# Performance work log

Measured on AMD Instinct MI355X. Metric: run time of the kernel, lower is better.

## Reference

```python
import jax, jax.numpy as jnp
import numpy as np

NEG_FILL = -9.0e15


def setup_inputs() -> dict:
    key = jax.random.key(0)
    k1, k2 = jax.random.split(key)
    z1 = jax.random.normal(k1, (4096, 256), dtype=jnp.float32)
    z2 = jax.random.normal(k2, (4096, 256), dtype=jnp.float32)
    return {"z1": z1, "z2": z2}


def reference(z1, z2, temperature=0.5):
    B = z1.shape[0]
    z = jnp.concatenate([z1, z2], axis=0)          # [2B, D]
    # cosine similarity == dot product of L2-normalized rows (torch eps=1e-8)
    norm = jnp.maximum(jnp.linalg.norm(z, axis=1, keepdims=True), 1e-8)
    zn = z / norm                                   # [2B, D]
    sim = (zn @ zn.T) / temperature                 # [2B, 2B]
    N = 2 * B
    eye = jnp.eye(N, dtype=bool)
    sim = jnp.where(eye, NEG_FILL, sim)
    idx = jnp.arange(N)
    # positives: (i, i+B mod 2B) -> diag(sim, B) then diag(sim, -B)
    pos_sim = sim[idx, (idx + B) % N]               # [2B]
    loss = -pos_sim + jax.nn.logsumexp(sim, axis=1)
    return jnp.mean(loss)
```

## Files before the change

### kernel.cpp

```cpp
#include <hip/hip_runtime.h>
#include <hip/hip_bf16.h>


typedef __attribute__((ext_vector_type(4))) float f32x4;
typedef __attribute__((ext_vector_type(8))) int i32x8;

#define N_TOT 8192
#define B_HALF 4096
#define D_DIM 256
#define JSPLIT 16
#define JCOLS 512
#define NSTEP 8
#define SCL_PRE 1.6986436f
#define RES_SCALE 0.6931471805599453f
#define S4 0x7B7B7B7B

__device__ inline float fexp2(float x) {
#if __has_builtin(__builtin_amdgcn_exp2f)
  return __builtin_amdgcn_exp2f(x);
#else
  return exp2f(x);
#endif
}

__device__ inline unsigned enc4(float v) {
  float av = fabsf(v);
  unsigned c = (av >= 0.25f) + (av >= 0.75f) + (av >= 1.25f) + (av >= 1.75f) +
               (av >= 2.5f) + (av >= 3.5f) + (av >= 5.0f);
  return c | ((v < 0.f) ? 8u : 0u);
}

__device__ inline i32x8 ld16z(const char* p) {
  int4 lo = *reinterpret_cast<const int4*>(p);
  i32x8 r = {lo.x, lo.y, lo.z, lo.w, 0, 0, 0, 0};
  return r;
}

__global__ __launch_bounds__(256) void nrm_kernel(const float* __restrict__ z1,
                                                  const float* __restrict__ z2,
                                                  unsigned short* __restrict__ zn4) {
  int row = blockIdx.x * 4 + (threadIdx.x >> 6);
  int lane = threadIdx.x & 63;
  const float* src = (row < B_HALF) ? (z1 + (size_t)row * D_DIM)
                                    : (z2 + (size_t)(row - B_HALF) * D_DIM);
  f32x4 v = *reinterpret_cast<const f32x4*>(src + lane * 4);
  float ss = v.x * v.x + v.y * v.y + v.z * v.z + v.w * v.w;
#pragma unroll
  for (int m = 32; m >= 1; m >>= 1) ss += __shfl_xor(ss, m);
  float inv = (SCL_PRE * 16.0f) / fmaxf(sqrtf(ss), 1e-8f);
  unsigned n0 = enc4(v.x * inv), n1 = enc4(v.y * inv);
  unsigned n2 = enc4(v.z * inv), n3 = enc4(v.w * inv);
  zn4[(size_t)row * 64 + lane] =
      (unsigned short)(n0 | (n1 << 4) | (n2 << 8) | (n3 << 12));
}

__global__ __launch_bounds__(256, 4) void gram_kernel(const unsigned short* __restrict__ zn4,
                                                      float* __restrict__ psum,
                                                      float* __restrict__ ppos) {
  __shared__ __align__(16) char bt[2 * 64 * 128];
  const int tid = threadIdx.x;
  const int w = tid >> 6, l = tid & 63;
  const int lm = l & 15, hh = l >> 4;
  const int r0w = blockIdx.x * 128 + w * 32;
  const int jbase = blockIdx.y * JCOLS;
  const char* znb = reinterpret_cast<const char*>(zn4);

  auto stage = [&](int s, int bi) {
    const char* gs = znb + (size_t)(jbase + s * 64) * 128;
    char* base = bt + bi * 8192 + w * 1024;
#pragma unroll
    for (int q = 0; q < 2; ++q) {
      int rloc = q * 32 + w * 8 + (l >> 3);
      int d = l & 7;
      const char* g = gs + (size_t)rloc * 128 + ((d ^ (rloc & 7)) << 4);
      __builtin_amdgcn_global_load_lds(
          (const __attribute__((address_space(1))) void*)g,
          (__attribute__((address_space(3))) void*)(base + q * 4096), 16, 0, 0);
    }
  };

  stage(0, 0);

  i32x8 a[2][2];
#pragma unroll
  for (int rf = 0; rf < 2; ++rf)
#pragma unroll
    for (int sl = 0; sl < 2; ++sl)
      a[rf][sl] = ld16z(znb + (size_t)(r0w + rf * 16 + lm) * 128 + sl * 64 + hh * 16);

  float sume[2][4];
#pragma unroll
  for (int rf = 0; rf < 2; ++rf)
#pragma unroll
    for (int t = 0; t < 4; ++t) sume[rf][t] = 0.f;

  const int swz = (lm & 7) << 4;

  f32x4 acA[2], acB[2];
  int pjtb = -1;

  auto readS = [&](const char* bp, int jt, int sl, i32x8& b) {
    const char* row = bp + (jt * 16 + lm) * 128;
    int cs = (sl * 64 + hh * 16) ^ swz;
    b = ld16z(row + cs);
  };

  auto epilogue = [&](const f32x4 (&pa)[2], int jtb) {
#pragma unroll
    for (int rf = 0; rf < 2; ++rf) {
      const int itb = r0w + rf * 16;
      const bool dg = (itb == jtb);
      const bool ps = ((itb ^ B_HALF) == jtb);
      if (dg | ps) {
#pragma unroll
        for (int t = 0; t < 4; ++t) {
          float sv = pa[rf][t];
          float e = fexp2(sv);
          bool self = (lm == hh * 4 + t);
          if (dg && self) e = 0.f;
          sume[rf][t] += e;
          if (ps && self) ppos[itb + hh * 4 + t] = sv * RES_SCALE;
        }
      } else {
#pragma unroll
        for (int t = 0; t < 4; ++t) sume[rf][t] += fexp2(pa[rf][t]);
      }
    }
  };

  auto mfma2 = [&](f32x4 (&acc)[2], const i32x8& b, int sl) {
    __builtin_amdgcn_s_setprio(1);
#pragma unroll
    for (int rf = 0; rf < 2; ++rf)
      acc[rf] = __builtin_amdgcn_mfma_scale_f32_16x16x128_f8f6f4(
          a[rf][sl], b, acc[rf], 4, 4, 0, S4, 0, S4);
    __builtin_amdgcn_s_setprio(0);
  };

  for (int s = 0; s < NSTEP; ++s) {
    __syncthreads();
    if (s + 1 < NSTEP) stage(s + 1, (s + 1) & 1);
    const char* bp = bt + (s & 1) * 8192;

    i32x8 b[8];
#pragma unroll
    for (int u = 0; u < 8; ++u) readS(bp, u >> 1, u & 1, b[u]);

#pragma unroll
    for (int jt = 0; jt < 4; ++jt) {
      f32x4(&acc)[2] = (jt & 1) ? acB : acA;
      f32x4(&prev)[2] = (jt & 1) ? acA : acB;

      if (pjtb >= 0) epilogue(prev, pjtb);
#pragma unroll
      for (int rf = 0; rf < 2; ++rf) acc[rf] = (f32x4){0.f, 0.f, 0.f, 0.f};
      mfma2(acc, b[jt * 2], 0);
      mfma2(acc, b[jt * 2 + 1], 1);
      pjtb = jbase + s * 64 + jt * 16;
    }
  }
  epilogue(acB, pjtb);

#pragma unroll
  for (int rf = 0; rf < 2; ++rf)
#pragma unroll
    for (int t = 0; t < 4; ++t) {
      float v = sume[rf][t];
#pragma unroll
      for (int m = 1; m < 16; m <<= 1) v += __shfl_xor(v, m);
      if (lm == 0) psum[(size_t)blockIdx.y * N_TOT + r0w + rf * 16 + hh * 4 + t] = v;
    }
}

__global__ __launch_bounds__(256) void fin1_kernel(const float* __restrict__ psum,
                                                   const float* __restrict__ ppos,
                                                   float* __restrict__ partial) {
  int i = blockIdx.x * 256 + threadIdx.x;
  float se = 0.f;
#pragma unroll
  for (int s = 0; s < JSPLIT; ++s) se += psum[(size_t)s * N_TOT + i];
  float acc = logf(se) - ppos[i];
#pragma unroll
  for (int m = 32; m >= 1; m >>= 1) acc += __shfl_xor(acc, m);
  __shared__ float red[4];
  if ((threadIdx.x & 63) == 0) red[threadIdx.x >> 6] = acc;
  __syncthreads();
  if (threadIdx.x == 0) partial[blockIdx.x] = red[0] + red[1] + red[2] + red[3];
}

__global__ void fin2_kernel(const float* __restrict__ partial, float* __restrict__ out) {
  float v = (threadIdx.x < 32) ? partial[threadIdx.x] : 0.f;
#pragma unroll
  for (int m = 32; m >= 1; m >>= 1) v += __shfl_xor(v, m);
  if (threadIdx.x == 0) out[0] = v / (float)N_TOT;
}

extern "C" void kernel_launch(void* const* d_in, const int* in_sizes, int n_in,
                              void* d_out, int out_size, void* d_ws, size_t ws_size,
                              hipStream_t stream) {
  const float* z1 = (const float*)d_in[0];
  const float* z2 = (const float*)d_in[1];
  float* out = (float*)d_out;
  char* ws = (char*)d_ws;

  unsigned short* zn4 = (unsigned short*)ws;
  float* psum = (float*)(ws + (size_t)N_TOT * 128);
  float* ppos = psum + (size_t)JSPLIT * N_TOT;
  float* partial = ppos + N_TOT;

  nrm_kernel<<<N_TOT / 4, 256, 0, stream>>>(z1, z2, zn4);
  gram_kernel<<<dim3(N_TOT / 128, JSPLIT), 256, 0, stream>>>(zn4, psum, ppos);
  fin1_kernel<<<N_TOT / 256, 256, 0, stream>>>(psum, ppos, partial);
  fin2_kernel<<<1, 64, 0, stream>>>(partial, out);
}
```

Measured before the change: 30.08 us.

## Exploit Gram matrix symmetry by computing only upper-triangular tiles

Restructures the gram kernel to compute only upper-triangular 128x256 tiles of the symmetric similarity matrix. Each exp value is added to both the row sum and a column sum, with column partials reduced through shared memory. The grid becomes a 1D triangular enumeration, and the finalize step gathers row and column partials. This roughly halves the MFMA and exp work, at the cost of extra column reductions, LDS traffic, a triangular index mapping, and uneven handling of the diagonal blocks.

New measurement: 43.18 us. 43.6% more time.

```diff
diff --git a/kernel.cpp b/kernel.cpp
--- a/kernel.cpp
+++ b/kernel.cpp
@@ -8,9 +8,10 @@
 #define N_TOT 8192
 #define B_HALF 4096
 #define D_DIM 256
-#define JSPLIT 16
-#define JCOLS 512
-#define NSTEP 8
+#define NROWP 32
+#define NCOLP 64
+#define NSTEP 4
+#define NBLK 1056
 #define SCL_PRE 1.6986436f
 #define RES_SCALE 0.6931471805599453f
 #define S4 0x7B7B7B7B
@@ -55,19 +56,32 @@
 }
 
 __global__ __launch_bounds__(256, 4) void gram_kernel(const unsigned short* __restrict__ zn4,
-                                                      float* __restrict__ psum,
+                                                      float* __restrict__ rowp,
+                                                      float* __restrict__ colp,
                                                       float* __restrict__ ppos) {
   __shared__ __align__(16) char bt[2 * 64 * 128];
+  __shared__ float colLDS[4][256];
   const int tid = threadIdx.x;
   const int w = tid >> 6, l = tid & 63;
   const int lm = l & 15, hh = l >> 4;
-  const int r0w = blockIdx.x * 128 + w * 32;
-  const int jbase = blockIdx.y * JCOLS;
+
+  const int L = blockIdx.x;
+  int p = (int)((65.0f - sqrtf(4225.0f - 4.0f * (float)L)) * 0.5f);
+  if (p < 0) p = 0;
+  while (p < 32 && (p + 1) * (65 - (p + 1)) <= L) ++p;
+  while (p > 0 && p * (65 - p) > L) --p;
+  int r = L - p * (65 - p);
+  int bi, bj;
+  if (r < 32 - p) { bi = 2 * p; bj = p + r; }
+  else            { bi = 2 * p + 1; bj = p + (r - (32 - p)); }
+
+  const int r0w = bi * 128 + w * 32;
+  const int jbase = bj * 256;
   const char* znb = reinterpret_cast<const char*>(zn4);
 
-  auto stage = [&](int s, int bi) {
+  auto stage = [&](int s, int bfi) {
     const char* gs = znb + (size_t)(jbase + s * 64) * 128;
-    char* base = bt + bi * 8192 + w * 1024;
+    char* base = bt + bfi * 8192 + w * 1024;
 #pragma unroll
     for (int q = 0; q < 2; ++q) {
       int rloc = q * 32 + w * 8 + (l >> 3);
@@ -96,70 +110,120 @@
 
   const int swz = (lm & 7) << 4;
 
-  f32x4 acA[2], acB[2];
-  int pjtb = -1;
-
   auto readS = [&](const char* bp, int jt, int sl, i32x8& b) {
     const char* row = bp + (jt * 16 + lm) * 128;
     int cs = (sl * 64 + hh * 16) ^ swz;
     b = ld16z(row + cs);
   };
 
-  auto epilogue = [&](const f32x4 (&pa)[2], int jtb) {
-#pragma unroll
-    for (int rf = 0; rf < 2; ++rf) {
-      const int itb = r0w + rf * 16;
-      const bool dg = (itb == jtb);
-      const bool ps = ((itb ^ B_HALF) == jtb);
-      if (dg | ps) {
+  if (bj > (bi >> 1)) {
+    f32x4 acA[2], acB[2];
+    int pjtb = -1, pcol = 0;
+
+    auto epiF = [&](const f32x4 (&pa)[2], int jtb, int pc) {
+      float csum = 0.f;
+#pragma unroll
+      for (int rf = 0; rf < 2; ++rf) {
+        const int itb = r0w + rf * 16;
+        const bool ps = ((itb ^ B_HALF) == jtb);
 #pragma unroll
         for (int t = 0; t < 4; ++t) {
           float sv = pa[rf][t];
           float e = fexp2(sv);
-          bool self = (lm == hh * 4 + t);
-          if (dg && self) e = 0.f;
           sume[rf][t] += e;
-          if (ps && self) ppos[itb + hh * 4 + t] = sv * RES_SCALE;
-        }
-      } else {
-#pragma unroll
-        for (int t = 0; t < 4; ++t) sume[rf][t] += fexp2(pa[rf][t]);
+          csum += e;
+          if (ps && (lm == hh * 4 + t)) {
+            ppos[itb + hh * 4 + t] = sv * RES_SCALE;
+            ppos[jtb + lm] = sv * RES_SCALE;
+          }
+        }
       }
-    }
-  };
-
-  auto mfma2 = [&](f32x4 (&acc)[2], const i32x8& b, int sl) {
-    __builtin_amdgcn_s_setprio(1);
-#pragma unroll
-    for (int rf = 0; rf < 2; ++rf)
-      acc[rf] = __builtin_amdgcn_mfma_scale_f32_16x16x128_f8f6f4(
-          a[rf][sl], b, acc[rf], 4, 4, 0, S4, 0, S4);
-    __builtin_amdgcn_s_setprio(0);
-  };
-
-  for (int s = 0; s < NSTEP; ++s) {
-    __syncthreads();
-    if (s + 1 < NSTEP) stage(s + 1, (s + 1) & 1);
-    const char* bp = bt + (s & 1) * 8192;
-
-    i32x8 b[8];
-#pragma unroll
-    for (int u = 0; u < 8; ++u) readS(bp, u >> 1, u & 1, b[u]);
-
-#pragma unroll
-    for (int jt = 0; jt < 4; ++jt) {
-      f32x4(&acc)[2] = (jt & 1) ? acB : acA;
-      f32x4(&prev)[2] = (jt & 1) ? acA : acB;
-
-      if (pjtb >= 0) epilogue(prev, pjtb);
-#pragma unroll
-      for (int rf = 0; rf < 2; ++rf) acc[rf] = (f32x4){0.f, 0.f, 0.f, 0.f};
-      mfma2(acc, b[jt * 2], 0);
-      mfma2(acc, b[jt * 2 + 1], 1);
-      pjtb = jbase + s * 64 + jt * 16;
+      csum += __shfl_xor(csum, 16);
+      csum += __shfl_xor(csum, 32);
+      if (hh == 0) colLDS[w][pc + lm] = csum;
+    };
+
+    for (int s = 0; s < NSTEP; ++s) {
+      __syncthreads();
+      if (s + 1 < NSTEP) stage(s + 1, (s + 1) & 1);
+      const char* bp = bt + (s & 1) * 8192;
+      i32x8 b[8];
+#pragma unroll
+      for (int u = 0; u < 8; ++u) readS(bp, u >> 1, u & 1, b[u]);
+
+#pragma unroll
+      for (int jt = 0; jt < 4; ++jt) {
+        f32x4(&acc)[2] = (jt & 1) ? acB : acA;
+        f32x4(&prev)[2] = (jt & 1) ? acA : acB;
+        if (pjtb >= 0) epiF(prev, pjtb, pcol);
+#pragma unroll
+        for (int rf = 0; rf < 2; ++rf) acc[rf] = (f32x4){0.f, 0.f, 0.f, 0.f};
+        __builtin_amdgcn_s_setprio(1);
+#pragma unroll
+        for (int rf = 0; rf < 2; ++rf) {
+          acc[rf] = __builtin_amdgcn_mfma_scale_f32_16x16x128_f8f6f4(
+              a[rf][0], b[jt * 2], acc[rf], 4, 4, 0, S4, 0, S4);
+          acc[rf] = __builtin_amdgcn_mfma_scale_f32_16x16x128_f8f6f4(
+              a[rf][1], b[jt * 2 + 1], acc[rf], 4, 4, 0, S4, 0, S4);
+        }
+        __builtin_amdgcn_s_setprio(0);
+        pjtb = jbase + s * 64 + jt * 16;
+        pcol = s * 64 + jt * 16;
+      }
+    }
+    epiF(acB, pjtb, pcol);
+  } else {
+    for (int s = 0; s < NSTEP; ++s) {
+      __syncthreads();
+      if (s + 1 < NSTEP) stage(s + 1, (s + 1) & 1);
+      const char* bp = bt + (s & 1) * 8192;
+      i32x8 b[8];
+#pragma unroll
+      for (int u = 0; u < 8; ++u) readS(bp, u >> 1, u & 1, b[u]);
+
+#pragma unroll
+      for (int jt = 0; jt < 4; ++jt) {
+        const int jtb = jbase + s * 64 + jt * 16;
+        float csum = 0.f;
+        f32x4 acc[2];
+#pragma unroll
+        for (int rf = 0; rf < 2; ++rf) acc[rf] = (f32x4){0.f, 0.f, 0.f, 0.f};
+#pragma unroll
+        for (int rf = 0; rf < 2; ++rf) {
+          const int itb = r0w + rf * 16;
+          if (jtb >= itb) {
+            acc[rf] = __builtin_amdgcn_mfma_scale_f32_16x16x128_f8f6f4(
+                a[rf][0], b[jt * 2], acc[rf], 4, 4, 0, S4, 0, S4);
+            acc[rf] = __builtin_amdgcn_mfma_scale_f32_16x16x128_f8f6f4(
+                a[rf][1], b[jt * 2 + 1], acc[rf], 4, 4, 0, S4, 0, S4);
+          }
+        }
+#pragma unroll
+        for (int rf = 0; rf < 2; ++rf) {
+          const int itb = r0w + rf * 16;
+          if (jtb < itb) continue;
+          if (jtb == itb) {
+#pragma unroll
+            for (int t = 0; t < 4; ++t) {
+              float e = fexp2(acc[rf][t]);
+              if (lm == hh * 4 + t) e = 0.f;
+              sume[rf][t] += e;
+            }
+          } else {
+#pragma unroll
+            for (int t = 0; t < 4; ++t) {
+              float e = fexp2(acc[rf][t]);
+              sume[rf][t] += e;
+              csum += e;
+            }
+          }
+        }
+        csum += __shfl_xor(csum, 16);
+        csum += __shfl_xor(csum, 32);
+        if (hh == 0) colLDS[w][s * 64 + jt * 16 + lm] = csum;
+      }
     }
   }
-  epilogue(acB, pjtb);
 
 #pragma unroll
   for (int rf = 0; rf < 2; ++rf)
@@ -168,24 +232,30 @@
       float v = sume[rf][t];
 #pragma unroll
       for (int m = 1; m < 16; m <<= 1) v += __shfl_xor(v, m);
-      if (lm == 0) psum[(size_t)blockIdx.y * N_TOT + r0w + rf * 16 + hh * 4 + t] = v;
-    }
-}
-
-__global__ __launch_bounds__(256) void fin1_kernel(const float* __restrict__ psum,
+      if (lm == 0) rowp[(size_t)bj * N_TOT + r0w + rf * 16 + hh * 4 + t] = v;
+    }
+
+  __syncthreads();
+  float cs = colLDS[0][tid] + colLDS[1][tid] + colLDS[2][tid] + colLDS[3][tid];
+  colp[(size_t)bi * N_TOT + jbase + tid] = cs;
+}
+
+__global__ __launch_bounds__(256) void fin1_kernel(const float* __restrict__ rowp,
+                                                   const float* __restrict__ colp,
                                                    const float* __restrict__ ppos,
                                                    float* __restrict__ partial) {
-  int i = blockIdx.x * 256 + threadIdx.x;
+  const int bx = blockIdx.x;
+  const int i = bx * 256 + threadIdx.x;
   float se = 0.f;
-#pragma unroll
-  for (int s = 0; s < JSPLIT; ++s) se += psum[(size_t)s * N_TOT + i];
+  for (int s = bx; s < NROWP; ++s) se += rowp[(size_t)s * N_TOT + i];
+  for (int s = 0; s <= 2 * bx + 1; ++s) se += colp[(size_t)s * N_TOT + i];
   float acc = logf(se) - ppos[i];
 #pragma unroll
   for (int m = 32; m >= 1; m >>= 1) acc += __shfl_xor(acc, m);
   __shared__ float red[4];
   if ((threadIdx.x & 63) == 0) red[threadIdx.x >> 6] = acc;
   __syncthreads();
-  if (threadIdx.x == 0) partial[blockIdx.x] = red[0] + red[1] + red[2] + red[3];
+  if (threadIdx.x == 0) partial[bx] = red[0] + red[1] + red[2] + red[3];
 }
 
 __global__ void fin2_kernel(const float* __restrict__ partial, float* __restrict__ out) {
@@ -204,12 +274,13 @@
   char* ws = (char*)d_ws;
 
   unsigned short* zn4 = (unsigned short*)ws;
-  float* psum = (float*)(ws + (size_t)N_TOT * 128);
-  float* ppos = psum + (size_t)JSPLIT * N_TOT;
+  float* rowp = (float*)(ws + (size_t)N_TOT * 128);
+  float* colp = rowp + (size_t)NROWP * N_TOT;
+  float* ppos = colp + (size_t)NCOLP * N_TOT;
   float* partial = ppos + N_TOT;
 
   nrm_kernel<<<N_TOT / 4, 256, 0, stream>>>(z1, z2, zn4);
-  gram_kernel<<<dim3(N_TOT / 128, JSPLIT), 256, 0, stream>>>(zn4, psum, ppos);
-  fin1_kernel<<<N_TOT / 256, 256, 0, stream>>>(psum, ppos, partial);
+  gram_kernel<<<NBLK, 256, 0, stream>>>(zn4, rowp, colp, ppos);
+  fin1_kernel<<<N_TOT / 256, 256, 0, stream>>>(rowp, colp, ppos, partial);
   fin2_kernel<<<1, 64, 0, stream>>>(partial, out);
 }
```

## Switch gram kernel from 16x16x128 to 32x32x64 scaled FP4 MFMA tiles

Applied to the files above, without the earlier changes.

Replaces the pairs of 16x16x128 scaled MFMAs per warp with a single 32x32x64 scaled MFMA tile. Each warp's 32 rows now form one 32x32 output tile, accumulated over four K-slices. The A and B fragment loads, the swizzled LDS reads, the epilogue row mapping and the shuffle reduction are re-derived for the 32-lane layout. The aim is to cut the instruction count and improve operand reuse per MFMA. In exchange there are larger accumulators, more register pressure, and less interleaving between the epilogue and the MFMAs.

Result: slower. 31.51 us (+4.8%).

```diff
diff --git a/kernel.cpp b/kernel.cpp
--- a/kernel.cpp
+++ b/kernel.cpp
@@ -3,6 +3,7 @@
 
 
 typedef __attribute__((ext_vector_type(4))) float f32x4;
+typedef __attribute__((ext_vector_type(16))) float f32x16;
 typedef __attribute__((ext_vector_type(8))) int i32x8;
 
 #define N_TOT 8192
@@ -60,14 +61,14 @@
   __shared__ __align__(16) char bt[2 * 64 * 128];
   const int tid = threadIdx.x;
   const int w = tid >> 6, l = tid & 63;
-  const int lm = l & 15, hh = l >> 4;
+  const int lm2 = l & 31, hh2 = l >> 5;
   const int r0w = blockIdx.x * 128 + w * 32;
   const int jbase = blockIdx.y * JCOLS;
   const char* znb = reinterpret_cast<const char*>(zn4);
 
-  auto stage = [&](int s, int bi) {
+  auto stage = [&](int s, int bfi) {
     const char* gs = znb + (size_t)(jbase + s * 64) * 128;
-    char* base = bt + bi * 8192 + w * 1024;
+    char* base = bt + bfi * 8192 + w * 1024;
 #pragma unroll
     for (int q = 0; q < 2; ++q) {
       int rloc = q * 32 + w * 8 + (l >> 3);
@@ -81,59 +82,52 @@
 
   stage(0, 0);
 
-  i32x8 a[2][2];
-#pragma unroll
-  for (int rf = 0; rf < 2; ++rf)
-#pragma unroll
-    for (int sl = 0; sl < 2; ++sl)
-      a[rf][sl] = ld16z(znb + (size_t)(r0w + rf * 16 + lm) * 128 + sl * 64 + hh * 16);
-
-  float sume[2][4];
-#pragma unroll
-  for (int rf = 0; rf < 2; ++rf)
-#pragma unroll
-    for (int t = 0; t < 4; ++t) sume[rf][t] = 0.f;
-
-  const int swz = (lm & 7) << 4;
-
-  f32x4 acA[2], acB[2];
+  i32x8 a[4];
+#pragma unroll
+  for (int sl = 0; sl < 4; ++sl)
+    a[sl] = ld16z(znb + (size_t)(r0w + lm2) * 128 + sl * 32 + hh2 * 16);
+
+  float sume[16];
+#pragma unroll
+  for (int t = 0; t < 16; ++t) sume[t] = 0.f;
+
+  const int swz = (lm2 & 7) << 4;
+
+  f32x16 acA, acB;
   int pjtb = -1;
 
   auto readS = [&](const char* bp, int jt, int sl, i32x8& b) {
-    const char* row = bp + (jt * 16 + lm) * 128;
-    int cs = (sl * 64 + hh * 16) ^ swz;
+    const char* row = bp + (jt * 32 + lm2) * 128;
+    int cs = (sl * 32 + hh2 * 16) ^ swz;
     b = ld16z(row + cs);
   };
 
-  auto epilogue = [&](const f32x4 (&pa)[2], int jtb) {
-#pragma unroll
-    for (int rf = 0; rf < 2; ++rf) {
-      const int itb = r0w + rf * 16;
-      const bool dg = (itb == jtb);
-      const bool ps = ((itb ^ B_HALF) == jtb);
-      if (dg | ps) {
-#pragma unroll
-        for (int t = 0; t < 4; ++t) {
-          float sv = pa[rf][t];
-          float e = fexp2(sv);
-          bool self = (lm == hh * 4 + t);
-          if (dg && self) e = 0.f;
-          sume[rf][t] += e;
-          if (ps && self) ppos[itb + hh * 4 + t] = sv * RES_SCALE;
-        }
-      } else {
-#pragma unroll
-        for (int t = 0; t < 4; ++t) sume[rf][t] += fexp2(pa[rf][t]);
+  auto epilogue = [&](const f32x16& pa, int jtb) {
+    const bool dg = (r0w == jtb);
+    const bool ps = ((r0w ^ B_HALF) == jtb);
+    if (dg | ps) {
+#pragma unroll
+      for (int t = 0; t < 16; ++t) {
+        float sv = pa[t];
+        float e = fexp2(sv);
+        int crow = (t & 3) + 8 * (t >> 2) + 4 * hh2;
+        bool self = (lm2 == crow);
+        if (dg && self) e = 0.f;
+        sume[t] += e;
+        if (ps && self) ppos[r0w + crow] = sv * RES_SCALE;
       }
+    } else {
+#pragma unroll
+      for (int t = 0; t < 16; ++t) sume[t] += fexp2(pa[t]);
     }
   };
 
-  auto mfma2 = [&](f32x4 (&acc)[2], const i32x8& b, int sl) {
+  auto mfma_tile = [&](f32x16& acc, const i32x8* b) {
     __builtin_amdgcn_s_setprio(1);
 #pragma unroll
-    for (int rf = 0; rf < 2; ++rf)
-      acc[rf] = __builtin_amdgcn_mfma_scale_f32_16x16x128_f8f6f4(
-          a[rf][sl], b, acc[rf], 4, 4, 0, S4, 0, S4);
+    for (int sl = 0; sl < 4; ++sl)
+      acc = __builtin_amdgcn_mfma_scale_f32_32x32x64_f8f6f4(
+          a[sl], b[sl], acc, 4, 4, 0, S4, 0, S4);
     __builtin_amdgcn_s_setprio(0);
   };
 
@@ -144,32 +138,31 @@
 
     i32x8 b[8];
 #pragma unroll
-    for (int u = 0; u < 8; ++u) readS(bp, u >> 1, u & 1, b[u]);
-
-#pragma unroll
-    for (int jt = 0; jt < 4; ++jt) {
-      f32x4(&acc)[2] = (jt & 1) ? acB : acA;
-      f32x4(&prev)[2] = (jt & 1) ? acA : acB;
-
-      if (pjtb >= 0) epilogue(prev, pjtb);
-#pragma unroll
-      for (int rf = 0; rf < 2; ++rf) acc[rf] = (f32x4){0.f, 0.f, 0.f, 0.f};
-      mfma2(acc, b[jt * 2], 0);
-      mfma2(acc, b[jt * 2 + 1], 1);
-      pjtb = jbase + s * 64 + jt * 16;
+    for (int u = 0; u < 8; ++u) readS(bp, u >> 2, u & 3, b[u]);
+
+    if (pjtb >= 0) epilogue(acB, pjtb);
+    acA = (f32x16){0.f, 0.f, 0.f, 0.f, 0.f, 0.f, 0.f, 0.f,
+                   0.f, 0.f, 0.f, 0.f, 0.f, 0.f, 0.f, 0.f};
+    mfma_tile(acA, &b[0]);
+
+    epilogue(acA, jbase + s * 64);
+    acB = (f32x16){0.f, 0.f, 0.f, 0.f, 0.f, 0.f, 0.f, 0.f,
+                   0.f, 0.f, 0.f, 0.f, 0.f, 0.f, 0.f, 0.f};
+    mfma_tile(acB, &b[4]);
+    pjtb = jbase + s * 64 + 32;
+  }
+  epilogue(acB, pjtb);
+
+#pragma unroll
+  for (int t = 0; t < 16; ++t) {
+    float v = sume[t];
+#pragma unroll
+    for (int m = 1; m < 32; m <<= 1) v += __shfl_xor(v, m);
+    if (lm2 == 0) {
+      int crow = (t & 3) + 8 * (t >> 2) + 4 * hh2;
+      psum[(size_t)blockIdx.y * N_TOT + r0w + crow] = v;
     }
   }
-  epilogue(acB, pjtb);
-
-#pragma unroll
-  for (int rf = 0; rf < 2; ++rf)
-#pragma unroll
-    for (int t = 0; t < 4; ++t) {
-      float v = sume[rf][t];
-#pragma unroll
-      for (int m = 1; m < 16; m <<= 1) v += __shfl_xor(v, m);
-      if (lm == 0) psum[(size_t)blockIdx.y * N_TOT + r0w + rf * 16 + hh * 4 + t] = v;
-    }
 }
 
 __global__ __launch_bounds__(256) void fin1_kernel(const float* __restrict__ psum,
```
